# Performance work log

Measured on AMD Instinct MI355X. Metric: run time of the kernel, lower is better.

The kernel has to match this reference:

```python
import jax, jax.numpy as jnp
import numpy as np

L = 9            # number of levels
T = 2097152      # entries per level (table has L*T rows)
F = 2            # features per entry
DOM_LO, DOM_HI = -1.0, 1.0
DOM_LEN = DOM_HI - DOM_LO
P = 262144       # number of query points


def setup_inputs() -> dict:
    key = jax.random.key(0)
    k1, k2 = jax.random.split(key)
    # points strictly inside the domain (-1, 1)
    x = jax.random.uniform(k1, (P, 3), jnp.float32) * 1.98 + (DOM_LO + 0.01)
    table = jax.random.normal(k2, (L * T, F), jnp.float32)  # nn.Embedding default N(0,1)
    return {"x": x, "table": table}


# 8 voxel-corner offsets, same order as the torch module
_OFFSETS = np.array([[0, 0, 0], [1, 0, 0], [0, 1, 0], [1, 1, 0],
                     [0, 0, 1], [1, 0, 1], [0, 1, 1], [1, 1, 1]], dtype=np.float32)


def reference(x, table):
    vs_f = jnp.float32(2.0) ** jnp.arange(L, dtype=jnp.float32)      # [L] voxel_size per level
    vs_i = (2 ** jnp.arange(L)).astype(jnp.int32)                    # [L] int version

    # points -> per-level grid space: [L, P, 3]
    norm = (x - DOM_LO) / DOM_LEN
    g = norm[None, :, :] * vs_f[:, None, None]
    base = jnp.floor(g)                                              # [L, P, 3]

    offs = jnp.asarray(_OFFSETS)                                     # [8, 3]
    corners = base[:, :, None, :] + offs[None, None, :, :]           # [L, P, 8, 3]
    grid_idx = corners.astype(jnp.int32)

    # corner positions back in world space: [L, P, 8, 3]
    grid_pos = corners / vs_f[:, None, None, None] * DOM_LEN + DOM_LO

    # flat embedding index: gx + gy*vs + gz*vs^2 (no hashing, as in source)
    flat = (grid_idx[..., 0]
            + grid_idx[..., 1] * vs_i[:, None, None]
            + grid_idx[..., 2] * (vs_i[:, None, None] ** 2))          # [L, P, 8] int32
    q = table[flat]                                                   # [L, P, 8, F]

    px, py, pz = x[:, 0], x[:, 1], x[:, 2]                            # each [P], broadcast over L
    x1, x2 = grid_pos[:, :, 0, 0], grid_pos[:, :, 1, 0]
    y1, y2 = grid_pos[:, :, 0, 1], grid_pos[:, :, 2, 1]
    z1, z2 = grid_pos[:, :, 0, 2], grid_pos[:, :, 4, 2]

    wx0 = ((x2 - px) / (x2 - x1))[..., None]                          # [L, P, 1]
    wx1 = ((px - x1) / (x2 - x1))[..., None]
    fx0 = wx0 * q[:, :, 0] + wx1 * q[:, :, 1]
    fx1 = wx0 * q[:, :, 2] + wx1 * q[:, :, 3]
    fx2 = wx0 * q[:, :, 4] + wx1 * q[:, :, 5]
    fx3 = wx0 * q[:, :, 6] + wx1 * q[:, :, 7]

    wy0 = ((y2 - py) / (y2 - y1))[..., None]
    wy1 = ((py - y1) / (y2 - y1))[..., None]
    fy0 = wy0 * fx0 + wy1 * fx1
    fy1 = wy0 * fx2 + wy1 * fx3

    wz0 = ((z2 - pz) / (z2 - z1))[..., None]
    wz1 = ((pz - z1) / (z2 - z1))[..., None]
    fz = wz0 * fy0 + wz1 * fy1                                        # [L, P, F]

    return jnp.transpose(fz, (1, 0, 2)).reshape(x.shape[0], L * F)    # [P, L*F]
```

## Files before the change

kernel.cpp:

```cpp
#include <hip/hip_runtime.h>

#define NLVL 9
#define NPTS 262144

__global__ __launch_bounds__(256) void hashgrid_enc_kernel(
    const float* __restrict__ x,
    const float* __restrict__ table,
    float* __restrict__ out)
{
    const int tid = blockIdx.x * blockDim.x + threadIdx.x;
    if (tid >= NPTS * NLVL) return;
    const int p = tid / NLVL;
    const int l = tid - p * NLVL;

    const float px = x[p * 3 + 0];
    const float py = x[p * 3 + 1];
    const float pz = x[p * 3 + 2];

    const int   s  = 1 << l;
    const float vs = (float)s;

    const float gx = (px + 1.0f) * 0.5f * vs;
    const float gy = (py + 1.0f) * 0.5f * vs;
    const float gz = (pz + 1.0f) * 0.5f * vs;

    const float bxf = floorf(gx);
    const float byf = floorf(gy);
    const float bzf = floorf(gz);

    const int ix = (int)bxf;
    const int iy = (int)byf;
    const int iz = (int)bzf;

    const float tx = gx - bxf;
    const float ty = gy - byf;
    const float tz = gz - bzf;
    const float ux = 1.0f - tx;
    const float uy = 1.0f - ty;
    const float uz = 1.0f - tz;

    const int s2   = s * s;
    const int f000 = ix + iy * s + iz * s2;

    const float2* __restrict__ tb = (const float2*)table;

    const float2 q0 = tb[f000];
    const float2 q1 = tb[f000 + 1];
    const float2 q2 = tb[f000 + s];
    const float2 q3 = tb[f000 + s + 1];
    const float2 q4 = tb[f000 + s2];
    const float2 q5 = tb[f000 + s2 + 1];
    const float2 q6 = tb[f000 + s2 + s];
    const float2 q7 = tb[f000 + s2 + s + 1];

    const float fx0a = ux * q0.x + tx * q1.x;
    const float fx0b = ux * q0.y + tx * q1.y;
    const float fx1a = ux * q2.x + tx * q3.x;
    const float fx1b = ux * q2.y + tx * q3.y;
    const float fx2a = ux * q4.x + tx * q5.x;
    const float fx2b = ux * q4.y + tx * q5.y;
    const float fx3a = ux * q6.x + tx * q7.x;
    const float fx3b = ux * q6.y + tx * q7.y;

    const float fy0a = uy * fx0a + ty * fx1a;
    const float fy0b = uy * fx0b + ty * fx1b;
    const float fy1a = uy * fx2a + ty * fx3a;
    const float fy1b = uy * fx2b + ty * fx3b;

    float2 r;
    r.x = uz * fy0a + tz * fy1a;
    r.y = uz * fy0b + tz * fy1b;

    ((float2*)out)[tid] = r;
}

extern "C" void kernel_launch(void* const* d_in, const int* in_sizes, int n_in,
                              void* d_out, int out_size, void* d_ws, size_t ws_size,
                              hipStream_t stream) {
    const float* x     = (const float*)d_in[0];
    const float* table = (const float*)d_in[1];
    float* out = (float*)d_out;

    const int total  = NPTS * NLVL;
    const int block  = 256;
    const int grid   = (total + block - 1) / block;
    hashgrid_enc_kernel<<<grid, block, 0, stream>>>(x, table, out);
}
```

Baseline: 240.6 us.

## Sort query points into Morton-ordered spatial buckets before grid gather

Adds a counting-sort pre-pass: a histogram over 4096 Morton-coded spatial buckets, a single-block scan, and a scatter that builds a permutation of the points. The encoding kernel then handles points in bucket order, so neighbouring threads gather nearby table entries and cache locality improves at the fine levels. In exchange it adds three kernel launches, a memset and atomics. The x loads and output writes become scattered, and points within a bucket end up in nondeterministic order.

```diff
diff --git a/kernel.cpp b/kernel.cpp
--- a/kernel.cpp
+++ b/kernel.cpp
@@ -1,17 +1,82 @@
 #include <hip/hip_runtime.h>
 
-#define NLVL 9
-#define NPTS 262144
+#define NLVL  9
+#define NPTS  262144
+#define NBUCK 4096
+
+#define WS_HIST(ws)   ((unsigned*)(ws))
+#define WS_OFFS(ws)   ((unsigned*)((char*)(ws) + 16384))
+#define WS_BUCKET(ws) ((unsigned*)((char*)(ws) + 32768))
+#define WS_PERM(ws)   ((unsigned*)((char*)(ws) + 32768 + (NPTS * 4)))
+
+__device__ __forceinline__ unsigned part3_4(unsigned v) {
+    v &= 0xFu;
+    v = (v | (v << 4)) & 0x0C3u;
+    v = (v | (v << 2)) & 0x249u;
+    return v;
+}
+
+__device__ __forceinline__ unsigned bucket_of(float px, float py, float pz) {
+    int bx = (int)((px + 1.0f) * 8.0f);
+    int by = (int)((py + 1.0f) * 8.0f);
+    int bz = (int)((pz + 1.0f) * 8.0f);
+    bx = min(max(bx, 0), 15); by = min(max(by, 0), 15); bz = min(max(bz, 0), 15);
+    return part3_4((unsigned)bx) | (part3_4((unsigned)by) << 1) | (part3_4((unsigned)bz) << 2);
+}
+
+__global__ __launch_bounds__(256) void hist_kernel(
+    const float* __restrict__ x, unsigned* __restrict__ hist, unsigned* __restrict__ bucket)
+{
+    const int p = blockIdx.x * blockDim.x + threadIdx.x;
+    if (p >= NPTS) return;
+    const unsigned b = bucket_of(x[p * 3 + 0], x[p * 3 + 1], x[p * 3 + 2]);
+    bucket[p] = b;
+    atomicAdd(&hist[b], 1u);
+}
+
+__global__ __launch_bounds__(256) void scan_kernel(
+    const unsigned* __restrict__ hist, unsigned* __restrict__ offs)
+{
+    __shared__ unsigned sums[256];
+    const int t = threadIdx.x;
+    unsigned local[16];
+    unsigned s = 0;
+    #pragma unroll
+    for (int i = 0; i < 16; ++i) { local[i] = hist[t * 16 + i]; s += local[i]; }
+    sums[t] = s;
+    __syncthreads();
+    for (int d = 1; d < 256; d <<= 1) {
+        unsigned add = (t >= d) ? sums[t - d] : 0u;
+        __syncthreads();
+        sums[t] += add;
+        __syncthreads();
+    }
+    unsigned excl = (t == 0) ? 0u : sums[t - 1];
+    #pragma unroll
+    for (int i = 0; i < 16; ++i) { offs[t * 16 + i] = excl; excl += local[i]; }
+}
+
+__global__ __launch_bounds__(256) void scatter_kernel(
+    const unsigned* __restrict__ bucket, unsigned* __restrict__ offs, unsigned* __restrict__ perm)
+{
+    const int p = blockIdx.x * blockDim.x + threadIdx.x;
+    if (p >= NPTS) return;
+    const unsigned b = bucket[p];
+    const unsigned pos = atomicAdd(&offs[b], 1u);
+    perm[pos] = (unsigned)p;
+}
 
 __global__ __launch_bounds__(256) void hashgrid_enc_kernel(
     const float* __restrict__ x,
     const float* __restrict__ table,
+    const unsigned* __restrict__ perm,
     float* __restrict__ out)
 {
     const int tid = blockIdx.x * blockDim.x + threadIdx.x;
     if (tid >= NPTS * NLVL) return;
-    const int p = tid / NLVL;
-    const int l = tid - p * NLVL;
+    const int sp = tid / NLVL;
+    const int l  = tid - sp * NLVL;
+    const int p  = (int)perm[sp];
 
     const float px = x[p * 3 + 0];
     const float py = x[p * 3 + 1];
@@ -71,7 +136,7 @@
     r.x = uz * fy0a + tz * fy1a;
     r.y = uz * fy0b + tz * fy1b;
 
-    ((float2*)out)[tid] = r;
+    ((float2*)out)[p * NLVL + l] = r;
 }
 
 extern "C" void kernel_launch(void* const* d_in, const int* in_sizes, int n_in,
@@ -81,8 +146,18 @@
     const float* table = (const float*)d_in[1];
     float* out = (float*)d_out;
 
-    const int total  = NPTS * NLVL;
-    const int block  = 256;
-    const int grid   = (total + block - 1) / block;
-    hashgrid_enc_kernel<<<grid, block, 0, stream>>>(x, table, out);
+    unsigned* hist   = WS_HIST(d_ws);
+    unsigned* offs   = WS_OFFS(d_ws);
+    unsigned* bucket = WS_BUCKET(d_ws);
+    unsigned* perm   = WS_PERM(d_ws);
+
+    hipMemsetAsync(hist, 0, NBUCK * sizeof(unsigned), stream);
+
+    const int pb = 256;
+    hist_kernel<<<(NPTS + pb - 1) / pb, pb, 0, stream>>>(x, hist, bucket);
+    scan_kernel<<<1, 256, 0, stream>>>(hist, offs);
+    scatter_kernel<<<(NPTS + pb - 1) / pb, pb, 0, stream>>>(bucket, offs, perm);
+
+    const int total = NPTS * NLVL;
+    hashgrid_enc_kernel<<<(total + pb - 1) / pb, pb, 0, stream>>>(x, table, perm, out);
 }
```

Result: slower. 279.5 us (+16.2%).

## Process all levels per thread instead of one thread per point-level

Applied to the files above, without the earlier changes.

Changes the work decomposition so each thread handles one point and loops over all nine levels, computing the normalized coordinates once and writing nine float2 results contiguously. This removes redundant point loads and the integer division, and gives each thread 72 independent gathers in flight. In exchange it launches nine times fewer threads, which reduces occupancy and parallelism for a gather-bound kernel. Output writes become strided across threads, which hurts coalescing.

```diff
diff --git a/kernel.cpp b/kernel.cpp
--- a/kernel.cpp
+++ b/kernel.cpp
@@ -3,75 +3,83 @@
 #define NLVL 9
 #define NPTS 262144
 
-__global__ __launch_bounds__(256) void hashgrid_enc_kernel(
+__global__ __launch_bounds__(256) void enc_kernel(
     const float* __restrict__ x,
     const float* __restrict__ table,
     float* __restrict__ out)
 {
-    const int tid = blockIdx.x * blockDim.x + threadIdx.x;
-    if (tid >= NPTS * NLVL) return;
-    const int p = tid / NLVL;
-    const int l = tid - p * NLVL;
+    const int p = blockIdx.x * blockDim.x + threadIdx.x;
+    if (p >= NPTS) return;
 
     const float px = x[p * 3 + 0];
     const float py = x[p * 3 + 1];
     const float pz = x[p * 3 + 2];
 
-    const int   s  = 1 << l;
-    const float vs = (float)s;
-
-    const float gx = (px + 1.0f) * 0.5f * vs;
-    const float gy = (py + 1.0f) * 0.5f * vs;
-    const float gz = (pz + 1.0f) * 0.5f * vs;
-
-    const float bxf = floorf(gx);
-    const float byf = floorf(gy);
-    const float bzf = floorf(gz);
-
-    const int ix = (int)bxf;
-    const int iy = (int)byf;
-    const int iz = (int)bzf;
-
-    const float tx = gx - bxf;
-    const float ty = gy - byf;
-    const float tz = gz - bzf;
-    const float ux = 1.0f - tx;
-    const float uy = 1.0f - ty;
-    const float uz = 1.0f - tz;
-
-    const int s2   = s * s;
-    const int f000 = ix + iy * s + iz * s2;
+    const float nx = (px + 1.0f) * 0.5f;
+    const float ny = (py + 1.0f) * 0.5f;
+    const float nz = (pz + 1.0f) * 0.5f;
 
     const float2* __restrict__ tb = (const float2*)table;
 
-    const float2 q0 = tb[f000];
-    const float2 q1 = tb[f000 + 1];
-    const float2 q2 = tb[f000 + s];
-    const float2 q3 = tb[f000 + s + 1];
-    const float2 q4 = tb[f000 + s2];
-    const float2 q5 = tb[f000 + s2 + 1];
-    const float2 q6 = tb[f000 + s2 + s];
-    const float2 q7 = tb[f000 + s2 + s + 1];
+    float2 res[NLVL];
 
-    const float fx0a = ux * q0.x + tx * q1.x;
-    const float fx0b = ux * q0.y + tx * q1.y;
-    const float fx1a = ux * q2.x + tx * q3.x;
-    const float fx1b = ux * q2.y + tx * q3.y;
-    const float fx2a = ux * q4.x + tx * q5.x;
-    const float fx2b = ux * q4.y + tx * q5.y;
-    const float fx3a = ux * q6.x + tx * q7.x;
-    const float fx3b = ux * q6.y + tx * q7.y;
+    #pragma unroll
+    for (int l = 0; l < NLVL; ++l) {
+        const int   s  = 1 << l;
+        const float vs = (float)s;
 
-    const float fy0a = uy * fx0a + ty * fx1a;
-    const float fy0b = uy * fx0b + ty * fx1b;
-    const float fy1a = uy * fx2a + ty * fx3a;
-    const float fy1b = uy * fx2b + ty * fx3b;
+        const float gx = nx * vs;
+        const float gy = ny * vs;
+        const float gz = nz * vs;
 
-    float2 r;
-    r.x = uz * fy0a + tz * fy1a;
-    r.y = uz * fy0b + tz * fy1b;
+        const float bxf = floorf(gx);
+        const float byf = floorf(gy);
+        const float bzf = floorf(gz);
 
-    ((float2*)out)[tid] = r;
+        const int ix = (int)bxf;
+        const int iy = (int)byf;
+        const int iz = (int)bzf;
+
+        const float tx = gx - bxf;
+        const float ty = gy - byf;
+        const float tz = gz - bzf;
+        const float ux = 1.0f - tx;
+        const float uy = 1.0f - ty;
+        const float uz = 1.0f - tz;
+
+        const int s2   = s * s;
+        const int f000 = ix + iy * s + iz * s2;
+
+        const float2 q0 = tb[f000];
+        const float2 q1 = tb[f000 + 1];
+        const float2 q2 = tb[f000 + s];
+        const float2 q3 = tb[f000 + s + 1];
+        const float2 q4 = tb[f000 + s2];
+        const float2 q5 = tb[f000 + s2 + 1];
+        const float2 q6 = tb[f000 + s2 + s];
+        const float2 q7 = tb[f000 + s2 + s + 1];
+
+        const float fx0a = ux * q0.x + tx * q1.x;
+        const float fx0b = ux * q0.y + tx * q1.y;
+        const float fx1a = ux * q2.x + tx * q3.x;
+        const float fx1b = ux * q2.y + tx * q3.y;
+        const float fx2a = ux * q4.x + tx * q5.x;
+        const float fx2b = ux * q4.y + tx * q5.y;
+        const float fx3a = ux * q6.x + tx * q7.x;
+        const float fx3b = ux * q6.y + tx * q7.y;
+
+        const float fy0a = uy * fx0a + ty * fx1a;
+        const float fy0b = uy * fx0b + ty * fx1b;
+        const float fy1a = uy * fx2a + ty * fx3a;
+        const float fy1b = uy * fx2b + ty * fx3b;
+
+        res[l].x = uz * fy0a + tz * fy1a;
+        res[l].y = uz * fy0b + tz * fy1b;
+    }
+
+    float2* o = (float2*)out + (size_t)p * NLVL;
+    #pragma unroll
+    for (int l = 0; l < NLVL; ++l) o[l] = res[l];
 }
 
 extern "C" void kernel_launch(void* const* d_in, const int* in_sizes, int n_in,
@@ -81,8 +89,7 @@
     const float* table = (const float*)d_in[1];
     float* out = (float*)d_out;
 
-    const int total  = NPTS * NLVL;
-    const int block  = 256;
-    const int grid   = (total + block - 1) / block;
-    hashgrid_enc_kernel<<<grid, block, 0, stream>>>(x, table, out);
+    const int block = 256;
+    const int grid  = (NPTS + block - 1) / block;
+    enc_kernel<<<grid, block, 0, stream>>>(x, table, out);
 }
```

After: 243.9 us. Within noise of the previous version (+1.4%).
